# Optimization experiments

Hardware: AMD Instinct MI355X
Metric: run time of the kernel (lower is better)

Reference implementation:

```python
import jax, jax.numpy as jnp
import numpy as np

NHEAD = 16

def setup_inputs() -> dict:
    key = jax.random.key(0)
    ks = jax.random.split(key, 7)
    b, l, d = 4, 2048, 1024
    s = 1.0 / np.sqrt(d)
    return {
        "Q": jax.random.normal(ks[0], (b, l, d), jnp.float32),
        "K": jax.random.normal(ks[1], (b, l, d), jnp.float32),
        "V": jax.random.normal(ks[2], (b, l, d), jnp.float32),
        "WQ": jax.random.normal(ks[3], (d, d), jnp.float32) * s,
        "WK": jax.random.normal(ks[4], (d, d), jnp.float32) * s,
        "WV": jax.random.normal(ks[5], (d, d), jnp.float32) * s,
        "WO": jax.random.normal(ks[6], (d, d), jnp.float32) * s,
    }

def reference(Q, K, V, WQ, WK, WV, WO):
    # WQ/WK/WV/WO stored torch-style as [out, in]; Linear(x) = x @ W.T
    b, lq, d = Q.shape
    lk = K.shape[1]
    h = NHEAD
    dk = d // h
    # project and split heads: [b, l, h, dk]
    q = (Q @ WQ.T).reshape(b, lq, h, dk)
    k = (K @ WK.T).reshape(b, lk, h, dk)
    v = (V @ WV.T).reshape(b, lk, h, dk)
    # scaled dot-product attention (dropout = identity in eval mode)
    scale = 1.0 / jnp.sqrt(jnp.asarray(dk, Q.dtype))
    score = jnp.einsum('bqhd,bkhd->bhqk', q, k) * scale  # [b,h,lq,lk]
    attn = jax.nn.softmax(score, axis=-1)
    o = jnp.einsum('bhqk,bkhd->bqhd', attn, v).reshape(b, lq, h * dk)
    return o @ WO.T
```

## Files before the change

kernel.cpp:

```cpp
#include <hip/hip_runtime.h>
#include <stdint.h>

#define D_MODEL 1024
#define NHEADS 16
#define DKH 64
#define SEQ 2048
#define BATCH 4
#define M_TOT (BATCH * SEQ)
#define LOG2E 1.44269504088896340736f

typedef __bf16 v8bf __attribute__((ext_vector_type(8)));
typedef __bf16 v4bf __attribute__((ext_vector_type(4)));
typedef _Float16 v8h __attribute__((ext_vector_type(8)));
typedef _Float16 v4h __attribute__((ext_vector_type(4)));
typedef float v4f __attribute__((ext_vector_type(4)));
typedef float v16f __attribute__((ext_vector_type(16)));
typedef unsigned int v4u __attribute__((ext_vector_type(4)));
typedef unsigned int v2u __attribute__((ext_vector_type(2)));

typedef const __attribute__((address_space(1))) void* gas_ptr;
typedef __attribute__((address_space(3))) void* las_ptr;

static __device__ __forceinline__ void async16(const void* g, void* l) {
    __builtin_amdgcn_global_load_lds((gas_ptr)g, (las_ptr)l, 16, 0, 0);
}

static __device__ __forceinline__ v4f mfma16x32(v8bf a, v8bf b, v4f c) {
    return __builtin_amdgcn_mfma_f32_16x16x32_bf16(a, b, c, 0, 0, 0);
}
static __device__ __forceinline__ v16f mfma32x16bf(v8bf a, v8bf b, v16f c) {
    return __builtin_amdgcn_mfma_f32_32x32x16_bf16(a, b, c, 0, 0, 0);
}
static __device__ __forceinline__ v16f mfma32x16h(v8h a, v8h b, v16f c) {
    return __builtin_amdgcn_mfma_f32_32x32x16_f16(a, b, c, 0, 0, 0);
}
static __device__ __forceinline__ unsigned pkh(float a, float b) {
    return __builtin_bit_cast(unsigned, __builtin_amdgcn_cvt_pkrtz(a, b));
}
static __device__ __forceinline__ void plswap(unsigned& x, unsigned& y) {
    v2u r = __builtin_amdgcn_permlane32_swap(x, y, false, false);
    x = r[0];
    y = r[1];
}
static __device__ __forceinline__ float fexp2(float x) {
#if __has_builtin(__builtin_amdgcn_exp2f)
    return __builtin_amdgcn_exp2f(x);
#else
    float r;
    asm("v_exp_f32 %0, %1" : "=v"(r) : "v"(x));
    return r;
#endif
}

__global__ __launch_bounds__(256) void cvt_x(const float* __restrict__ src,
                                             __bf16* __restrict__ dst) {
    int i = blockIdx.x * 256 + threadIdx.x;
    const float4* s = (const float4*)src;
    float4 a = s[2 * i], b = s[2 * i + 1];
    v8bf o;
    o[0] = (__bf16)a.x; o[1] = (__bf16)a.y; o[2] = (__bf16)a.z; o[3] = (__bf16)a.w;
    o[4] = (__bf16)b.x; o[5] = (__bf16)b.y; o[6] = (__bf16)b.z; o[7] = (__bf16)b.w;
    *(v8bf*)(dst + (size_t)i * 8) = o;
}

__global__ __launch_bounds__(256) void cvt_x3(const float* __restrict__ s0,
                                              const float* __restrict__ s1,
                                              const float* __restrict__ s2,
                                              __bf16* __restrict__ d0,
                                              __bf16* __restrict__ d1,
                                              __bf16* __restrict__ d2) {
    int t = blockIdx.x >> 12;
    int i = (blockIdx.x & 4095) * 256 + threadIdx.x;
    const float* src = (t == 0) ? s0 : (t == 1) ? s1 : s2;
    __bf16* dst = (t == 0) ? d0 : (t == 1) ? d1 : d2;
    const float4* s = (const float4*)src;
    float4 a = s[2 * i], b = s[2 * i + 1];
    v8bf o;
    o[0] = (__bf16)a.x; o[1] = (__bf16)a.y; o[2] = (__bf16)a.z; o[3] = (__bf16)a.w;
    o[4] = (__bf16)b.x; o[5] = (__bf16)b.y; o[6] = (__bf16)b.z; o[7] = (__bf16)b.w;
    *(v8bf*)(dst + (size_t)i * 8) = o;
}

__global__ __launch_bounds__(256) void cvt_w(const float* __restrict__ w0,
                                             const float* __restrict__ w1,
                                             const float* __restrict__ w2,
                                             const float* __restrict__ w3,
                                             __bf16* __restrict__ dst) {
    int gid = blockIdx.x * 256 + threadIdx.x;
    int tsel = gid >> 17;
    int off = gid & 131071;
    const float* s = (tsel == 0) ? w0 : (tsel == 1) ? w1 : (tsel == 2) ? w2 : w3;
    const float4* sp = (const float4*)s + 2 * (size_t)off;
    float4 a = sp[0], b = sp[1];
    v8bf o;
    o[0] = (__bf16)a.x; o[1] = (__bf16)a.y; o[2] = (__bf16)a.z; o[3] = (__bf16)a.w;
    o[4] = (__bf16)b.x; o[5] = (__bf16)b.y; o[6] = (__bf16)b.z; o[7] = (__bf16)b.w;
    *(v8bf*)(dst + ((size_t)tsel << 20) + (size_t)off * 8) = o;
}

template <int LAYOUT>
__global__ __launch_bounds__(256) void gemm_nt(const __bf16* __restrict__ A,
                                               const __bf16* __restrict__ W,
                                               void* __restrict__ Cv, float scale) {
    const int t = threadIdx.x, lane = t & 63, wave = t >> 6;
    const int r = lane & 15, qd = lane >> 4;
    const int m0 = blockIdx.x * 128, n0 = blockIdx.y * 128;
    const int mw = (wave & 1) * 64, nw = (wave >> 1) * 64;

    __shared__ __align__(16) __bf16 As[128 * 32];
    __shared__ __align__(16) __bf16 Bs[128 * 32];

    const int wc = (lane & 3) ^ ((lane >> 3) & 3);
    const int wrow = lane >> 2;
    const int rdpos = (qd ^ ((r >> 1) & 3)) * 8;

    v4f acc[4][4] = {};
    for (int k0 = 0; k0 < D_MODEL; k0 += 32) {
#pragma unroll
        for (int p = 0; p < 2; ++p) {
            int rb = (p * 4 + wave) * 16;
            async16(A + (size_t)(m0 + rb + wrow) * D_MODEL + k0 + wc * 8, &As[rb * 32]);
            async16(W + (size_t)(n0 + rb + wrow) * D_MODEL + k0 + wc * 8, &Bs[rb * 32]);
        }
        __syncthreads();
        v8bf af[4], bfr[4];
#pragma unroll
        for (int mt = 0; mt < 4; ++mt)
            af[mt] = *(const v8bf*)&As[(mw + mt * 16 + r) * 32 + rdpos];
#pragma unroll
        for (int nt = 0; nt < 4; ++nt)
            bfr[nt] = *(const v8bf*)&Bs[(nw + nt * 16 + r) * 32 + rdpos];
#pragma unroll
        for (int mt = 0; mt < 4; ++mt)
#pragma unroll
            for (int nt = 0; nt < 4; ++nt)
                acc[mt][nt] = mfma16x32(af[mt], bfr[nt], acc[mt][nt]);
        __syncthreads();
    }

#pragma unroll
    for (int mt = 0; mt < 4; ++mt)
#pragma unroll
        for (int nt = 0; nt < 4; ++nt) {
            int row = m0 + mw + mt * 16 + qd * 4;
            int col = n0 + nw + nt * 16 + r;
            if (LAYOUT == 0) {
                float* C = (float*)Cv;
#pragma unroll
                for (int i = 0; i < 4; ++i)
                    C[(size_t)(row + i) * D_MODEL + col] = acc[mt][nt][i];
            } else {
                int bb = row >> 11, l = row & (SEQ - 1);
                int h = col >> 6, d = col & (DKH - 1);
                if (LAYOUT == 2) {
                    _Float16* vt = (_Float16*)Cv;
                    v4h o;
#pragma unroll
                    for (int i = 0; i < 4; ++i) o[i] = (_Float16)acc[mt][nt][i];
                    *(v4h*)&vt[((size_t)((bb * NHEADS + h) * DKH + d)) * SEQ + l] = o;
                } else {
                    __bf16* dst = (__bf16*)Cv;
#pragma unroll
                    for (int i = 0; i < 4; ++i)
                        dst[(((size_t)(bb * NHEADS + h) * SEQ) + l + i) * DKH + d] =
                            (__bf16)(acc[mt][nt][i] * scale);
                }
            }
        }
}

__global__ __launch_bounds__(256) void gemm_qkv(const __bf16* __restrict__ xq,
                                                const __bf16* __restrict__ xk,
                                                const __bf16* __restrict__ xv,
                                                const __bf16* __restrict__ wb,
                                                __bf16* __restrict__ qh,
                                                __bf16* __restrict__ kh,
                                                _Float16* __restrict__ vtb, float qs) {
    const int z = blockIdx.z;
    const __bf16* A = (z == 0) ? xq : (z == 1) ? xk : xv;
    const __bf16* W = wb + (size_t)z * D_MODEL * D_MODEL;

    const int t = threadIdx.x, lane = t & 63, wave = t >> 6;
    const int r = lane & 15, qd = lane >> 4;
    const int m0 = blockIdx.x * 128, n0 = blockIdx.y * 128;
    const int mw = (wave & 1) * 64, nw = (wave >> 1) * 64;

    __shared__ __align__(16) __bf16 As[128 * 32];
    __shared__ __align__(16) __bf16 Bs[128 * 32];

    const int wc = (lane & 3) ^ ((lane >> 3) & 3);
    const int wrow = lane >> 2;
    const int rdpos = (qd ^ ((r >> 1) & 3)) * 8;

    v4f acc[4][4] = {};
    for (int k0 = 0; k0 < D_MODEL; k0 += 32) {
#pragma unroll
        for (int p = 0; p < 2; ++p) {
            int rb = (p * 4 + wave) * 16;
            async16(A + (size_t)(m0 + rb + wrow) * D_MODEL + k0 + wc * 8, &As[rb * 32]);
            async16(W + (size_t)(n0 + rb + wrow) * D_MODEL + k0 + wc * 8, &Bs[rb * 32]);
        }
        __syncthreads();
        v8bf af[4], bfr[4];
#pragma unroll
        for (int mt = 0; mt < 4; ++mt)
            af[mt] = *(const v8bf*)&As[(mw + mt * 16 + r) * 32 + rdpos];
#pragma unroll
        for (int nt = 0; nt < 4; ++nt)
            bfr[nt] = *(const v8bf*)&Bs[(nw + nt * 16 + r) * 32 + rdpos];
#pragma unroll
        for (int mt = 0; mt < 4; ++mt)
#pragma unroll
            for (int nt = 0; nt < 4; ++nt)
                acc[mt][nt] = mfma16x32(af[mt], bfr[nt], acc[mt][nt]);
        __syncthreads();
    }

    const float scale = (z == 0) ? qs : 1.0f;
#pragma unroll
    for (int mt = 0; mt < 4; ++mt)
#pragma unroll
        for (int nt = 0; nt < 4; ++nt) {
            int row = m0 + mw + mt * 16 + qd * 4;
            int col = n0 + nw + nt * 16 + r;
            int bb = row >> 11, l = row & (SEQ - 1);
            int h = col >> 6, d = col & (DKH - 1);
            if (z == 2) {
                v4h o;
#pragma unroll
                for (int i = 0; i < 4; ++i) o[i] = (_Float16)acc[mt][nt][i];
                *(v4h*)&vtb[((size_t)((bb * NHEADS + h) * DKH + d)) * SEQ + l] = o;
            } else {
                __bf16* dst = (z == 0) ? qh : kh;
#pragma unroll
                for (int i = 0; i < 4; ++i)
                    dst[(((size_t)(bb * NHEADS + h) * SEQ) + l + i) * DKH + d] =
                        (__bf16)(acc[mt][nt][i] * scale);
            }
        }
}

__global__ __launch_bounds__(256, 2) void attn_kernel(const __bf16* __restrict__ qh,
                                                      const __bf16* __restrict__ kh,
                                                      const _Float16* __restrict__ vt,
                                                      __bf16* __restrict__ oh) {
    const int lane = threadIdx.x & 63, wave = threadIdx.x >> 6;
    const int l31 = lane & 31, hi = lane >> 5, l7 = lane & 7;
    const int id = blockIdx.x;
    const int bh = (id & 7) * 8 + ((id >> 3) & 7);
    const int q0 = (id >> 6) * 256 + wave * 64;

    __shared__ __align__(16) __bf16 Kb[2][64 * 64];
    __shared__ __align__(16) _Float16 Vb[2][64 * 64];

    const __bf16* kbh = kh + (size_t)bh * SEQ * DKH;
    const _Float16* vbh = vt + (size_t)bh * DKH * SEQ;

    v8bf qf[2][4];
#pragma unroll
    for (int qa = 0; qa < 2; ++qa)
#pragma unroll
        for (int c = 0; c < 4; ++c)
            qf[qa][c] = *(const v8bf*)&qh[((size_t)bh * SEQ + q0 + qa * 32 + l31) * DKH +
                                          c * 16 + hi * 8];

    v16f oacc[2][2] = {};
    float ps[2] = {0.f, 0.f};
    const v16f dz = {};

    const int srow = lane >> 3;
    const int sc = (lane & 7) ^ srow;

#pragma unroll
    for (int p = 0; p < 2; ++p) {
        int rb = wave * 16 + p * 8;
        async16(kbh + (size_t)(rb + srow) * DKH + sc * 8, &Kb[0][rb * 64]);
        async16(vbh + (size_t)(rb + srow) * SEQ + sc * 8, &Vb[0][rb * 64]);
    }

    for (int tt = 0; tt < SEQ / 64; ++tt) {
        const int buf = tt & 1;
        __syncthreads();
        if (tt + 1 < SEQ / 64) {
            const int t0 = (tt + 1) * 64;
#pragma unroll
            for (int p = 0; p < 2; ++p) {
                int rb = wave * 16 + p * 8;
                async16(kbh + (size_t)(t0 + rb + srow) * DKH + sc * 8, &Kb[buf ^ 1][rb * 64]);
                async16(vbh + (size_t)(rb + srow) * SEQ + t0 + sc * 8, &Vb[buf ^ 1][rb * 64]);
            }
        }
        const __bf16* Kc = Kb[buf];
        const _Float16* Vc = Vb[buf];
#pragma unroll
        for (int kb = 0; kb < 2; ++kb) {
            v8bf ka[4];
#pragma unroll
            for (int c = 0; c < 4; ++c)
                ka[c] = *(const v8bf*)&Kc[(kb * 32 + l31) * 64 + (((c * 2 + hi) ^ l7) << 3)];
            v8h pb[2][2];
#pragma unroll
            for (int qa = 0; qa < 2; ++qa) {
                __builtin_amdgcn_s_setprio(1);
                v16f d = mfma32x16bf(ka[0], qf[qa][0], dz);
#pragma unroll
                for (int c = 1; c < 4; ++c) d = mfma32x16bf(ka[c], qf[qa][c], d);
                __builtin_amdgcn_s_setprio(0);
                float e[16];
#pragma unroll
                for (int i = 0; i < 16; ++i) e[i] = fexp2(d[i]);
                ps[qa] += (((e[0] + e[1]) + (e[2] + e[3])) + ((e[4] + e[5]) + (e[6] + e[7]))) +
                          (((e[8] + e[9]) + (e[10] + e[11])) + ((e[12] + e[13]) + (e[14] + e[15])));
#pragma unroll
                for (int kc = 0; kc < 2; ++kc) {
                    unsigned a0 = pkh(e[kc * 8 + 0], e[kc * 8 + 1]);
                    unsigned a1 = pkh(e[kc * 8 + 2], e[kc * 8 + 3]);
                    unsigned b0 = pkh(e[kc * 8 + 4], e[kc * 8 + 5]);
                    unsigned b1 = pkh(e[kc * 8 + 6], e[kc * 8 + 7]);
                    plswap(a0, b0);
                    plswap(a1, b1);
                    v4u w = {a0, a1, b0, b1};
                    pb[qa][kc] = __builtin_bit_cast(v8h, w);
                }
            }
            __builtin_amdgcn_s_setprio(1);
#pragma unroll
            for (int dg = 0; dg < 2; ++dg)
#pragma unroll
                for (int kc = 0; kc < 2; ++kc) {
                    v8h va = *(const v8h*)&Vc[(dg * 32 + l31) * 64 +
                                              (((kb * 4 + kc * 2 + hi) ^ l7) << 3)];
#pragma unroll
                    for (int qa = 0; qa < 2; ++qa)
                        oacc[qa][dg] = mfma32x16h(va, pb[qa][kc], oacc[qa][dg]);
                }
            __builtin_amdgcn_s_setprio(0);
        }
    }

    const int b = bh >> 4, h = bh & (NHEADS - 1);
#pragma unroll
    for (int qa = 0; qa < 2; ++qa) {
        float tot = ps[qa] + __shfl_xor(ps[qa], 32, 64);
        float inv = 1.0f / tot;
        int lq = q0 + qa * 32 + l31;
        __bf16* op = oh + (((size_t)(b * SEQ + lq)) * NHEADS + h) * DKH;
#pragma unroll
        for (int dg = 0; dg < 2; ++dg)
#pragma unroll
            for (int g = 0; g < 4; ++g) {
                v4bf ov;
#pragma unroll
                for (int i = 0; i < 4; ++i) ov[i] = (__bf16)(oacc[qa][dg][g * 4 + i] * inv);
                *(v4bf*)(op + dg * 32 + g * 8 + hi * 4) = ov;
            }
    }
}

extern "C" void kernel_launch(void* const* d_in, const int* in_sizes, int n_in,
                              void* d_out, int out_size, void* d_ws, size_t ws_size,
                              hipStream_t stream) {
    const float* Q = (const float*)d_in[0];
    const float* K = (const float*)d_in[1];
    const float* V = (const float*)d_in[2];
    const float* WQ = (const float*)d_in[3];
    const float* WK = (const float*)d_in[4];
    const float* WV = (const float*)d_in[5];
    const float* WO = (const float*)d_in[6];
    float* out = (float*)d_out;

    const size_t elems = (size_t)M_TOT * D_MODEL;
    const size_t welems = (size_t)D_MODEL * D_MODEL;
    const size_t fused_need = 8 * welems + 6 * 2 * elems;

    dim3 gg(M_TOT / 128, D_MODEL / 128);

    if (ws_size >= fused_need) {
        __bf16* wb = (__bf16*)d_ws;
        __bf16* xq = wb + 4 * welems;
        __bf16* xk = xq + elems;
        __bf16* xv = xk + elems;
        __bf16* qh = xv + elems;
        __bf16* kh = qh + elems;
        _Float16* vtb = (_Float16*)(kh + elems);
        __bf16* oh = xq;

        cvt_w<<<2048, 256, 0, stream>>>(WQ, WK, WV, WO, wb);
        cvt_x3<<<3 * 4096, 256, 0, stream>>>(Q, K, V, xq, xk, xv);
        dim3 gz(M_TOT / 128, D_MODEL / 128, 3);
        gemm_qkv<<<gz, 256, 0, stream>>>(xq, xk, xv, wb, qh, kh, vtb, 0.125f * LOG2E);
        attn_kernel<<<512, 256, 0, stream>>>(qh, kh, vtb, oh);
        gemm_nt<0><<<gg, 256, 0, stream>>>(oh, wb + 3 * welems, out, 1.0f);
    } else {
        __bf16* wb = (__bf16*)d_ws;
        __bf16* xb = wb + 4 * welems;
        __bf16* qh = xb + elems;
        __bf16* kh = qh + elems;
        _Float16* vtb = (_Float16*)(kh + elems);
        __bf16* oh = (__bf16*)(vtb + elems);

        cvt_w<<<2048, 256, 0, stream>>>(WQ, WK, WV, WO, wb);
        cvt_x<<<4096, 256, 0, stream>>>(Q, xb);
        gemm_nt<1><<<gg, 256, 0, stream>>>(xb, wb, qh, 0.125f * LOG2E);
        cvt_x<<<4096, 256, 0, stream>>>(K, xb);
        gemm_nt<1><<<gg, 256, 0, stream>>>(xb, wb + welems, kh, 1.0f);
        cvt_x<<<4096, 256, 0, stream>>>(V, xb);
        gemm_nt<2><<<gg, 256, 0, stream>>>(xb, wb + 2 * welems, vtb, 1.0f);
        attn_kernel<<<512, 256, 0, stream>>>(qh, kh, vtb, oh);
        gemm_nt<0><<<gg, 256, 0, stream>>>(oh, wb + 3 * welems, out, 1.0f);
    }
}
```

Before: 323.6 us.

## Double-buffer GEMM LDS tiles with async prefetch and drop attention setprio hints

The projection GEMM k-loops now use two LDS buffers. The next k-slice is issued with global_load_lds before computing on the current one, and partial vmcnt waits plus raw s_barrier replace the full __syncthreads. This is meant to hide global load latency behind MFMA work in the QKV and output projections. Separately, the s_setprio calls around the attention MFMAs are removed. The cost is doubled LDS per block, which may reduce occupancy.

```diff
diff --git a/kernel.cpp b/kernel.cpp
--- a/kernel.cpp
+++ b/kernel.cpp
@@ -98,6 +98,37 @@
     *(v8bf*)(dst + ((size_t)tsel << 20) + (size_t)off * 8) = o;
 }
 
+#define GEMM_KLOOP(Abase, Wbase)                                                   \
+    auto stage = [&](int bi, int k0) {                                             \
+        _Pragma("unroll") for (int p = 0; p < 2; ++p) {                            \
+            int rb = (p * 4 + wave) * 16;                                          \
+            async16(Abase + (size_t)(rb + wrow) * D_MODEL + k0, &As[bi][rb * 32]); \
+            async16(Wbase + (size_t)(rb + wrow) * D_MODEL + k0, &Bs[bi][rb * 32]); \
+        }                                                                          \
+    };                                                                             \
+    stage(0, 0);                                                                   \
+    for (int it = 0; it < D_MODEL / 32; ++it) {                                    \
+        const int cur = it & 1;                                                    \
+        if (it + 1 < D_MODEL / 32) {                                               \
+            stage(cur ^ 1, (it + 1) * 32);                                         \
+            asm volatile("s_waitcnt vmcnt(4)" ::: "memory");                       \
+        } else {                                                                   \
+            asm volatile("s_waitcnt vmcnt(0)" ::: "memory");                       \
+        }                                                                          \
+        __builtin_amdgcn_s_barrier();                                              \
+        __builtin_amdgcn_sched_barrier(0);                                         \
+        v8bf af[4], bfr[4];                                                        \
+        _Pragma("unroll") for (int mt = 0; mt < 4; ++mt)                           \
+            af[mt] = *(const v8bf*)&As[cur][(mw + mt * 16 + r) * 32 + rdpos];      \
+        _Pragma("unroll") for (int nt = 0; nt < 4; ++nt)                           \
+            bfr[nt] = *(const v8bf*)&Bs[cur][(nw + nt * 16 + r) * 32 + rdpos];     \
+        _Pragma("unroll") for (int mt = 0; mt < 4; ++mt)                           \
+            _Pragma("unroll") for (int nt = 0; nt < 4; ++nt)                       \
+                acc[mt][nt] = mfma16x32(af[mt], bfr[nt], acc[mt][nt]);             \
+        asm volatile("s_waitcnt lgkmcnt(0)" ::: "memory");                         \
+        __builtin_amdgcn_s_barrier();                                              \
+    }
+
 template <int LAYOUT>
 __global__ __launch_bounds__(256) void gemm_nt(const __bf16* __restrict__ A,
                                                const __bf16* __restrict__ W,
@@ -107,36 +138,18 @@
     const int m0 = blockIdx.x * 128, n0 = blockIdx.y * 128;
     const int mw = (wave & 1) * 64, nw = (wave >> 1) * 64;
 
-    __shared__ __align__(16) __bf16 As[128 * 32];
-    __shared__ __align__(16) __bf16 Bs[128 * 32];
+    __shared__ __align__(16) __bf16 As[2][128 * 32];
+    __shared__ __align__(16) __bf16 Bs[2][128 * 32];
 
     const int wc = (lane & 3) ^ ((lane >> 3) & 3);
     const int wrow = lane >> 2;
     const int rdpos = (qd ^ ((r >> 1) & 3)) * 8;
 
+    const __bf16* Ab = A + (size_t)m0 * D_MODEL + wc * 8;
+    const __bf16* Wb = W + (size_t)n0 * D_MODEL + wc * 8;
+
     v4f acc[4][4] = {};
-    for (int k0 = 0; k0 < D_MODEL; k0 += 32) {
-#pragma unroll
-        for (int p = 0; p < 2; ++p) {
-            int rb = (p * 4 + wave) * 16;
-            async16(A + (size_t)(m0 + rb + wrow) * D_MODEL + k0 + wc * 8, &As[rb * 32]);
-            async16(W + (size_t)(n0 + rb + wrow) * D_MODEL + k0 + wc * 8, &Bs[rb * 32]);
-        }
-        __syncthreads();
-        v8bf af[4], bfr[4];
-#pragma unroll
-        for (int mt = 0; mt < 4; ++mt)
-            af[mt] = *(const v8bf*)&As[(mw + mt * 16 + r) * 32 + rdpos];
-#pragma unroll
-        for (int nt = 0; nt < 4; ++nt)
-            bfr[nt] = *(const v8bf*)&Bs[(nw + nt * 16 + r) * 32 + rdpos];
-#pragma unroll
-        for (int mt = 0; mt < 4; ++mt)
-#pragma unroll
-            for (int nt = 0; nt < 4; ++nt)
-                acc[mt][nt] = mfma16x32(af[mt], bfr[nt], acc[mt][nt]);
-        __syncthreads();
-    }
+    GEMM_KLOOP(Ab, Wb)
 
 #pragma unroll
     for (int mt = 0; mt < 4; ++mt)
@@ -185,36 +198,18 @@
     const int m0 = blockIdx.x * 128, n0 = blockIdx.y * 128;
     const int mw = (wave & 1) * 64, nw = (wave >> 1) * 64;
 
-    __shared__ __align__(16) __bf16 As[128 * 32];
-    __shared__ __align__(16) __bf16 Bs[128 * 32];
+    __shared__ __align__(16) __bf16 As[2][128 * 32];
+    __shared__ __align__(16) __bf16 Bs[2][128 * 32];
 
     const int wc = (lane & 3) ^ ((lane >> 3) & 3);
     const int wrow = lane >> 2;
     const int rdpos = (qd ^ ((r >> 1) & 3)) * 8;
 
+    const __bf16* Ab = A + (size_t)m0 * D_MODEL + wc * 8;
+    const __bf16* Wb = W + (size_t)n0 * D_MODEL + wc * 8;
+
     v4f acc[4][4] = {};
-    for (int k0 = 0; k0 < D_MODEL; k0 += 32) {
-#pragma unroll
-        for (int p = 0; p < 2; ++p) {
-            int rb = (p * 4 + wave) * 16;
-            async16(A + (size_t)(m0 + rb + wrow) * D_MODEL + k0 + wc * 8, &As[rb * 32]);
-            async16(W + (size_t)(n0 + rb + wrow) * D_MODEL + k0 + wc * 8, &Bs[rb * 32]);
-        }
-        __syncthreads();
-        v8bf af[4], bfr[4];
-#pragma unroll
-        for (int mt = 0; mt < 4; ++mt)
-            af[mt] = *(const v8bf*)&As[(mw + mt * 16 + r) * 32 + rdpos];
-#pragma unroll
-        for (int nt = 0; nt < 4; ++nt)
-            bfr[nt] = *(const v8bf*)&Bs[(nw + nt * 16 + r) * 32 + rdpos];
-#pragma unroll
-        for (int mt = 0; mt < 4; ++mt)
-#pragma unroll
-            for (int nt = 0; nt < 4; ++nt)
-                acc[mt][nt] = mfma16x32(af[mt], bfr[nt], acc[mt][nt]);
-        __syncthreads();
-    }
+    GEMM_KLOOP(Ab, Wb)
 
     const float scale = (z == 0) ? qs : 1.0f;
 #pragma unroll
@@ -301,11 +296,9 @@
             v8h pb[2][2];
 #pragma unroll
             for (int qa = 0; qa < 2; ++qa) {
-                __builtin_amdgcn_s_setprio(1);
                 v16f d = mfma32x16bf(ka[0], qf[qa][0], dz);
 #pragma unroll
                 for (int c = 1; c < 4; ++c) d = mfma32x16bf(ka[c], qf[qa][c], d);
-                __builtin_amdgcn_s_setprio(0);
                 float e[16];
 #pragma unroll
                 for (int i = 0; i < 16; ++i) e[i] = fexp2(d[i]);
@@ -323,7 +316,6 @@
                     pb[qa][kc] = __builtin_bit_cast(v8h, w);
                 }
             }
-            __builtin_amdgcn_s_setprio(1);
 #pragma unroll
             for (int dg = 0; dg < 2; ++dg)
 #pragma unroll
@@ -334,7 +326,6 @@
                     for (int qa = 0; qa < 2; ++qa)
                         oacc[qa][dg] = mfma32x16h(va, pb[qa][kc], oacc[qa][dg]);
                 }
-            __builtin_amdgcn_s_setprio(0);
         }
     }
 
```

After: 323.2 us. Within noise of the previous version (-0.1%).
